# Kernel optimization log

Measured on AMD Instinct MI355X. Metric: run time of the kernel, lower is better.

## Reference

```python
import math
import jax, jax.numpy as jnp
import numpy as np

B_, L_, D_, N_, R_ = 4, 1024, 1024, 16, 64  # batch, seq, n_embd(=dim_inner), d_state, dt_rank


def setup_inputs() -> dict:
    key = jax.random.key(0)
    ks = jax.random.split(key, 6)
    s = lambda k, shp: jax.random.normal(k, shp, jnp.float32) * 0.02
    return {
        "x": jax.random.normal(ks[0], (B_, L_, D_), jnp.float32),
        "ln1_w": jnp.ones((D_,), jnp.float32),
        "ln2_w": jnp.ones((D_,), jnp.float32),
        "W_dbc": s(ks[1], (R_ + 2 * N_, D_)),   # x -> [delta_lowrank, B, C]
        "W_dt": s(ks[2], (D_, R_)),              # dt_rank -> dim_inner
        "b_dt": jnp.zeros((D_,), jnp.float32),
        "A_log": jnp.log(jnp.broadcast_to(jnp.arange(1, N_ + 1, dtype=jnp.float32), (D_, N_))),
        "Dp": jnp.ones((D_,), jnp.float32),      # skip-connection D parameter
        "W_fc": s(ks[3], (4 * D_, D_)),
        "W_proj": s(ks[4], (D_, 4 * D_)),
    }


def _layernorm(x, w):
    mu = jnp.mean(x, -1, keepdims=True)
    xc = x - mu
    var = jnp.mean(xc * xc, -1, keepdims=True)
    return xc * jax.lax.rsqrt(var + 1e-5) * w


def _new_gelu(x):
    c = math.sqrt(2.0 / math.pi)
    return 0.5 * x * (1.0 + jnp.tanh(c * (x + 0.044715 * x * x * x)))


def _ssm(x, W_dbc, W_dt, b_dt, A_log, Dp):
    # x: (b, l, d) with d == dim_inner == n_embd
    dbc = jnp.einsum("bld,ed->ble", x, W_dbc)                # (b,l,R+2N)
    delta, Bm, Cm = jnp.split(dbc, [R_, R_ + N_], axis=-1)
    delta = jax.nn.softplus(jnp.einsum("blr,dr->bld", delta, W_dt) + b_dt)  # (b,l,d)
    A = -jnp.exp(A_log)                                       # (d,n)
    dA = jnp.exp(delta[..., None] * A)                        # (b,l,d,n) discretized A
    dBx = (delta * x)[..., None] * Bm[:, :, None, :]          # (b,l,d,n) discretized B*x

    # h_t = dA_t * h_{t-1} + dBx_t  -> parallel first-order linear scan
    def combine(e1, e2):
        a1, b1 = e1
        a2, b2 = e2
        return a2 * a1, a2 * b1 + b2

    _, hs = jax.lax.associative_scan(combine, (dA, dBx), axis=1)
    y = jnp.einsum("bldn,bln->bld", hs, Cm)
    return y + x * Dp


def reference(x, ln1_w, ln2_w, W_dbc, W_dt, b_dt, A_log, Dp, W_fc, W_proj):
    h = jax.nn.softplus(_layernorm(x, ln1_w))
    h = h + _ssm(h, W_dbc, W_dt, b_dt, A_log, Dp)
    m = _layernorm(h, ln2_w)
    m = _new_gelu(jnp.einsum("bld,fd->blf", m, W_fc))
    m = jnp.einsum("blf,df->bld", m, W_proj)
    return h + m
```

## Files before the change

kernel.cpp:

```cpp
#include <hip/hip_runtime.h>
#include <cstdint>
#include <cstddef>

typedef unsigned short u16;
typedef unsigned int u32;
typedef __attribute__((ext_vector_type(8))) short short8;
typedef __attribute__((ext_vector_type(4))) float floatx4;
typedef __attribute__((ext_vector_type(4))) u16 u16x4;
typedef __attribute__((ext_vector_type(4))) u32 u32x4;

#define DEV static __device__ __forceinline__

DEV u16 f2b(float f){ u32 u = __float_as_uint(f); u32 r = u + 0x7fffu + ((u>>16)&1u); return (u16)(r>>16); }
DEV float softplusf(float z){ return fmaxf(z,0.f) + log1pf(__expf(-fabsf(z))); }
DEV float fast_tanhf(float u){ float e = __expf(2.f*u); return 1.f - 2.f/(e+1.f); }
DEV float geluf(float x){ float u = 0.7978845608028654f*(x + 0.044715f*x*x*x); return 0.5f*x*(1.f+fast_tanhf(u)); }

DEV void async_copy16(const void* gp, void* lp){
  __builtin_amdgcn_global_load_lds((const __attribute__((address_space(1))) u32*)gp,
                                   (__attribute__((address_space(3))) u32*)lp, 16, 0, 0);
}

DEV u32 ldsoff(const void* p){
  return (u32)(size_t)(const __attribute__((address_space(3))) char*)p;
}

DEV void ds_read128x4(u32 base, short8* dst){
  u32x4 r0, r1, r2, r3;
  asm volatile("ds_read_b128 %0, %4 offset:0\n\t"
               "ds_read_b128 %1, %4 offset:1024\n\t"
               "ds_read_b128 %2, %4 offset:2048\n\t"
               "ds_read_b128 %3, %4 offset:3072"
               : "=&v"(r0), "=&v"(r1), "=&v"(r2), "=&v"(r3)
               : "v"(base));
  union { u32x4 u; short8 s; } c0, c1, c2, c3;
  c0.u = r0; c1.u = r1; c2.u = r2; c3.u = r3;
  dst[0] = c0.s; dst[1] = c1.s; dst[2] = c2.s; dst[3] = c3.s;
}

__global__ __launch_bounds__(256)
void prep_ln1(const float* __restrict__ Wdbc, const float* __restrict__ Wdt,
              const float* __restrict__ Wfc, const float* __restrict__ Wproj,
              u16* __restrict__ dbc_b, u16* __restrict__ dt_b,
              u16* __restrict__ fc_b, u16* __restrict__ pj_b,
              const float* __restrict__ x, const float* __restrict__ ln1w,
              float* __restrict__ h0f, u16* __restrict__ h0b)
{
  __shared__ float red[8];
  int bx = blockIdx.x, tid = threadIdx.x;
  if (bx < 8384){
    int i = bx*256 + tid;
    const float* src; u16* dst; int j;
    if (i < 32768){
      int e = i*4, r = e >> 10;
      if (r >= 96){ u16x4 z = {0,0,0,0}; *(u16x4*)(dbc_b + e) = z; return; }
      src = Wdbc; dst = dbc_b; j = i;
    } else if (i < 49152){ src = Wdt;   dst = dt_b; j = i - 32768; }
    else if (i < 1097728){ src = Wfc;   dst = fc_b; j = i - 49152; }
    else                 { src = Wproj; dst = pj_b; j = i - 1097728; }
    float4 v = ((const float4*)src)[j];
    u16x4 o = { f2b(v.x), f2b(v.y), f2b(v.z), f2b(v.w) };
    *(u16x4*)(dst + j*4) = o;
    return;
  }
  int row = bx - 8384;
  const float4* xr = (const float4*)(x + (size_t)row*1024);
  float4 v = xr[tid];
  float s1 = v.x+v.y+v.z+v.w;
  float s2 = v.x*v.x+v.y*v.y+v.z*v.z+v.w*v.w;
  #pragma unroll
  for (int m=1;m<64;m<<=1){ s1 += __shfl_xor(s1,m); s2 += __shfl_xor(s2,m); }
  int wv = tid>>6;
  if ((tid&63)==0){ red[wv]=s1; red[4+wv]=s2; }
  __syncthreads();
  s1 = red[0]+red[1]+red[2]+red[3];
  s2 = red[4]+red[5]+red[6]+red[7];
  float mu  = s1*(1.f/1024.f);
  float var = s2*(1.f/1024.f) - mu*mu;
  float rstd = rsqrtf(var + 1e-5f);
  float4 wv4 = ((const float4*)ln1w)[tid];
  float o0 = softplusf((v.x-mu)*rstd*wv4.x);
  float o1 = softplusf((v.y-mu)*rstd*wv4.y);
  float o2 = softplusf((v.z-mu)*rstd*wv4.z);
  float o3 = softplusf((v.w-mu)*rstd*wv4.w);
  ((float4*)(h0f + (size_t)row*1024))[tid] = make_float4(o0,o1,o2,o3);
  u16x4 ob = { f2b(o0), f2b(o1), f2b(o2), f2b(o3) };
  *(u16x4*)(h0b + (size_t)row*1024 + tid*4) = ob;
}

__global__ void dbc_post(const float* __restrict__ p, u16* __restrict__ delta_in,
                         float* __restrict__ BCf){
  int e = blockIdx.x*256 + threadIdx.x;
  int t = e >> 7, c = e & 127;
  float s = 0.f;
  #pragma unroll
  for (int z=0;z<8;z++) s += p[(size_t)z*524288 + e];
  if (c < 64)      delta_in[t*64 + c] = f2b(s);
  else if (c < 96) BCf[t*32 + (c-64)] = s;
}

__global__ void proj_reduce(const float* __restrict__ p, float* __restrict__ out){
  int i = blockIdx.x*256 + threadIdx.x;
  float4 a = ((const float4*)p)[i];
  float4 b = ((const float4*)(p + (size_t) 4194304))[i];
  float4 c = ((const float4*)(p + (size_t) 8388608))[i];
  float4 d = ((const float4*)(p + (size_t)12582912))[i];
  float4 r = ((float4*)out)[i];
  float4 o = make_float4(a.x+b.x+c.x+d.x+r.x, a.y+b.y+c.y+d.y+r.y,
                         a.z+b.z+c.z+d.z+r.z, a.w+b.w+c.w+d.w+r.w);
  ((float4*)out)[i] = o;
}

__global__ __launch_bounds__(256)
void ln2_kernel(const float* __restrict__ x, const float* __restrict__ w,
                u16* __restrict__ outb)
{
  int row = blockIdx.x, tid = threadIdx.x;
  const float4* xr = (const float4*)(x + (size_t)row*1024);
  float4 v = xr[tid];
  float s1 = v.x+v.y+v.z+v.w;
  float s2 = v.x*v.x+v.y*v.y+v.z*v.z+v.w*v.w;
  #pragma unroll
  for (int m=1;m<64;m<<=1){ s1 += __shfl_xor(s1,m); s2 += __shfl_xor(s2,m); }
  __shared__ float red[8];
  int wv = tid>>6;
  if ((tid&63)==0){ red[wv]=s1; red[4+wv]=s2; }
  __syncthreads();
  s1 = red[0]+red[1]+red[2]+red[3];
  s2 = red[4]+red[5]+red[6]+red[7];
  float mu  = s1*(1.f/1024.f);
  float var = s2*(1.f/1024.f) - mu*mu;
  float rstd = rsqrtf(var + 1e-5f);
  float4 wv4 = ((const float4*)w)[tid];
  u16x4 ob = { f2b((v.x-mu)*rstd*wv4.x), f2b((v.y-mu)*rstd*wv4.y),
               f2b((v.z-mu)*rstd*wv4.z), f2b((v.w-mu)*rstd*wv4.w) };
  *(u16x4*)(outb + (size_t)row*1024 + tid*4) = ob;
}

template<int EPI, int SWZ>
__global__ __launch_bounds__(256)
void gemm_bt(const u16* __restrict__ A, int lda,
             const u16* __restrict__ B, int ldb, int K,
             float* __restrict__ outF, u16* __restrict__ outB, int ldo,
             const float* __restrict__ bias, size_t zstr)
{
  __shared__ u16 sA[128*32];
  __shared__ u16 sB[128*32];
  const int tid = threadIdx.x;
  int m_blk, n_blk, zb;
  if (SWZ == 0){ n_blk = blockIdx.x; m_blk = blockIdx.y; zb = blockIdx.z; }
  else if (SWZ == 1){
    int b = blockIdx.x, xcd = b & 7, local = b >> 3;
    m_blk = (xcd>>2)*16 + (local & 15);
    n_blk = (xcd&3)*8 + (local >> 4);
    zb = 0;
  } else {
    int b = blockIdx.x, xcd = b & 7, local = b >> 3;
    m_blk = (xcd>>1)*8 + (local & 7);
    n_blk = local >> 3;
    zb = xcd & 1;
  }
  const int m0 = m_blk*128, n0 = n_blk*128;
  const int kstart = zb * K;
  const int wave = tid>>6, lane = tid&63;
  const int wm = (wave>>1)*64, wn = (wave&1)*64;
  const int lr = lane&15, quad = lane>>4;

  floatx4 acc[4][4];
  #pragma unroll
  for (int i=0;i<4;i++)
    #pragma unroll
    for (int j=0;j<4;j++){ floatx4 z = {0.f,0.f,0.f,0.f}; acc[i][j]=z; }

  const int r0 = tid>>2;
  const int kc8 = (((tid&3) ^ ((tid>>3)&3)))*8;
  const int sswz = ((lr>>1)&3);
  for (int k0=kstart; k0<kstart+K; k0+=32){
    __syncthreads();
    async_copy16(A + (size_t)(m0+r0)*lda    + k0+kc8, &sA[(size_t)tid*8]);
    async_copy16(A + (size_t)(m0+64+r0)*lda + k0+kc8, &sA[(size_t)(tid+256)*8]);
    async_copy16(B + (size_t)(n0+r0)*ldb    + k0+kc8, &sB[(size_t)tid*8]);
    async_copy16(B + (size_t)(n0+64+r0)*ldb + k0+kc8, &sB[(size_t)(tid+256)*8]);
    __syncthreads();
    short8 af[4], bf[4];
    #pragma unroll
    for (int i=0;i<4;i++){
      af[i] = *(const short8*)&sA[(wm+i*16+lr)*32 + (quad^sswz)*8];
      bf[i] = *(const short8*)&sB[(wn+i*16+lr)*32 + (quad^sswz)*8];
    }
    #pragma unroll
    for (int i=0;i<4;i++)
      #pragma unroll
      for (int j=0;j<4;j++)
        acc[i][j] = __builtin_amdgcn_mfma_f32_16x16x32_bf16(af[i], bf[j], acc[i][j], 0,0,0);
  }
  #pragma unroll
  for (int i=0;i<4;i++){
    #pragma unroll
    for (int j=0;j<4;j++){
      #pragma unroll
      for (int r=0;r<4;r++){
        int gr = m0 + wm + i*16 + quad*4 + r;
        int gc = n0 + wn + j*16 + lr;
        float v = acc[i][j][r];
        size_t o = (size_t)gr*ldo + gc;
        if (EPI==1)      outF[o] = softplusf(v + bias[gc]);
        else if (EPI==2) outB[o] = f2b(geluf(v));
        else             outF[zstr*zb + o] = v;
      }
    }
  }
}

template<int EPI, int SWZ>
__global__ __launch_bounds__(512, 2)
void gemm256(const u16* __restrict__ A, int lda,
             const u16* __restrict__ B, int ldb, int K,
             float* __restrict__ outF, u16* __restrict__ outB, int ldo, size_t zstr)
{
  __shared__ u16 sA[2][4][4096];
  __shared__ u16 sB[2][4][4096];
  const int tid = threadIdx.x;
  int m_blk, n_blk, zb;
  if (SWZ == 3){
    int b = blockIdx.x, xcd = b & 7, local = b >> 3;
    m_blk = (xcd>>2)*8 + (local & 7);
    n_blk = (xcd&3)*4 + (local >> 3);
    zb = 0;
  } else {
    int b = blockIdx.x, xcd = b & 7, local = b >> 3;
    zb    = xcd >> 1;
    m_blk = (xcd&1)*8 + (local & 7);
    n_blk = local >> 3;
  }
  const int m0 = m_blk*256, n0 = n_blk*256;
  const int kstart = zb*K;
  const int wave = tid>>6, lane = tid&63;
  const int mq = wave>>2, nq = wave&3;
  const int lr = lane&15, quad = lane>>4;
  const int sswz = (lr>>1)&3;

  const int srow = tid>>2;
  const int scol = ((tid&3) ^ ((tid>>3)&3))*8;
  const u16* pa = A + (size_t)(m0 + srow)*lda + scol;
  const u16* pb = B + (size_t)(n0 + srow)*ldb + scol;
  u16* la = (u16*)sA + tid*8;
  u16* lb = (u16*)sB + tid*8;
  const size_t ah128 = (size_t)128*lda;
  const size_t bh128 = (size_t)128*ldb;

  const int a_rd = (mq*64 + lr)*32 + (quad^sswz)*8;
  const int b_rd = ((nq&1)*64 + lr)*32 + (quad^sswz)*8;
  const int bun  = nq>>1;
  const u32 a_rdB = ldsoff(sA) + (u32)(a_rd*2);
  const u32 b_rdB = ldsoff(sB) + (u32)(b_rd*2) + (u32)(bun*8192);

  floatx4 acc[2][4][4];
  #pragma unroll
  for (int h=0;h<2;h++)
    #pragma unroll
    for (int i=0;i<4;i++)
      #pragma unroll
      for (int j=0;j<4;j++){ floatx4 z={0.f,0.f,0.f,0.f}; acc[h][i][j]=z; }

  short8 af[2][4], bf[2][4];

#define STG_A(NB,KS,H,KT) async_copy16(pa + (size_t)(H)*ah128 + (size_t)((KT) + (KS)*32), \
                                       la + (NB)*16384 + ((KS)*2+(H))*4096)
#define STG_B(NB,KS,H,KT) async_copy16(pb + (size_t)(H)*bh128 + (size_t)((KT) + (KS)*32), \
                                       lb + (NB)*16384 + ((KS)*2+(H))*4096)

#define PH(MFS, MBS, AH, PRBUF, PRKS, PRAH, PRB, VM, LG, STMTS)               \
  {                                                                           \
    STMTS;                                                                    \
    asm volatile("s_waitcnt vmcnt(" VM ")" ::: "memory");                     \
    __builtin_amdgcn_s_barrier();                                             \
    ds_read128x4(a_rdB + (PRBUF)*32768u + (PRKS)*16384u + (PRAH)*8192u,       \
                 af[(MFS)^1]);                                                \
    if (PRB)                                                                  \
      ds_read128x4(b_rdB + (PRBUF)*32768u + (PRKS)*16384u, bf[(MBS)^1]);      \
    asm volatile("s_waitcnt lgkmcnt(" LG ")" ::: "memory");                   \
    __builtin_amdgcn_sched_barrier(0);                                        \
    __builtin_amdgcn_s_setprio(1);                                            \
    _Pragma("unroll")                                                         \
    for (int i_=0;i_<4;i_++)                                                  \
      _Pragma("unroll")                                                       \
      for (int j_=0;j_<4;j_++)                                                \
        acc[AH][i_][j_] = __builtin_amdgcn_mfma_f32_16x16x32_bf16(            \
            af[MFS][i_], bf[MBS][j_], acc[AH][i_][j_], 0,0,0);                \
    __builtin_amdgcn_s_setprio(0);                                            \
  }

  STG_A(0,0,0,kstart); STG_B(0,0,0,kstart);
  STG_B(0,0,1,kstart); STG_A(0,0,1,kstart);
  STG_B(0,1,0,kstart); STG_B(0,1,1,kstart);
  STG_A(0,1,0,kstart); STG_A(0,1,1,kstart);
  asm volatile("s_waitcnt vmcnt(5)" ::: "memory");
  __builtin_amdgcn_s_barrier();
  ds_read128x4(a_rdB, af[0]);
  ds_read128x4(b_rdB, bf[0]);

  const int NT = K >> 6;
  for (int t=0; t<NT; t+=2){
    const int ka = kstart + (t+1)*64;
    const int kb = (t+2 < NT) ? (kstart + (t+2)*64) : kstart;
    PH(0,0,0, 0,0,1,0, "6","4", STG_A(1,0,0,ka); STG_B(1,0,0,ka));
    PH(1,0,1, 0,1,0,1, "5","8", STG_B(1,0,1,ka); STG_A(1,0,1,ka));
    PH(0,1,0, 0,1,1,0, "6","4", STG_B(1,1,0,ka); STG_B(1,1,1,ka));
    PH(1,1,1, 1,0,0,1, "5","8", STG_A(1,1,0,ka); STG_A(1,1,1,ka));
    PH(0,0,0, 1,0,1,0, "6","4", STG_A(0,0,0,kb); STG_B(0,0,0,kb));
    PH(1,0,1, 1,1,0,1, "5","8", STG_B(0,0,1,kb); STG_A(0,0,1,kb));
    PH(0,1,0, 1,1,1,0, "6","4", STG_B(0,1,0,kb); STG_B(0,1,1,kb));
    PH(1,1,1, 0,0,0,1, "5","8", STG_A(0,1,0,kb); STG_A(0,1,1,kb));
  }

#undef PH
#undef STG_A
#undef STG_B

  #pragma unroll
  for (int h=0;h<2;h++){
    #pragma unroll
    for (int i=0;i<4;i++){
      #pragma unroll
      for (int j=0;j<4;j++){
        #pragma unroll
        for (int r=0;r<4;r++){
          int gr = m0 + h*128 + mq*64 + i*16 + quad*4 + r;
          int gc = n0 + nq*64 + j*16 + lr;
          float v = acc[h][i][j][r];
          size_t o = (size_t)gr*ldo + gc;
          if (EPI==2) outB[o] = f2b(geluf(v));
          else        outF[zstr*zb + o] = v;
        }
      }
    }
  }
}

__global__ __launch_bounds__(256)
void scan_p1(const float* __restrict__ delta, const float* __restrict__ h0f,
             const float* __restrict__ BCf, const float* __restrict__ A_log,
             float* __restrict__ Pbuf, float* __restrict__ Sbuf)
{
  int blk = blockIdx.x;
  int d = (blk & 3)*256 + threadIdx.x;
  int c = (blk >> 2) & 31;
  int b = blk >> 7;
  float a2[16], h[16], P[16];
  #pragma unroll
  for (int n=0;n<16;n++){ a2[n] = -__expf(A_log[d*16+n]) * 1.44269504f; h[n]=0.f; P[n]=1.f; }
  int t0 = c*32;
  const float* dptr = delta + ((size_t)(b*1024 + t0))*1024 + d;
  const float* xptr = h0f   + ((size_t)(b*1024 + t0))*1024 + d;
  const float* bc   = BCf   + ((size_t)(b*1024 + t0))*32;
  #pragma unroll 4
  for (int t=0;t<32;t++){
    float dlt = dptr[t*1024];
    float xv  = xptr[t*1024];
    float dx = dlt*xv;
    #pragma unroll
    for (int n=0;n<16;n++){
      float dA = exp2f(dlt*a2[n]);
      h[n] = dA*h[n] + dx*bc[t*32+n];
      P[n] *= dA;
    }
  }
  size_t base = ((size_t)((b*32 + c)*16))*1024 + d;
  #pragma unroll
  for (int n=0;n<16;n++){ Pbuf[base + (size_t)n*1024] = P[n]; Sbuf[base + (size_t)n*1024] = h[n]; }
}

__global__ __launch_bounds__(256)
void scan_p2(const float* __restrict__ Pbuf, const float* __restrict__ Sbuf,
             float* __restrict__ Hbuf)
{
  int blk = blockIdx.x;
  int d = (blk & 3)*256 + threadIdx.x;
  int n = (blk >> 2) & 15;
  int b = blk >> 6;
  float H = 0.f;
  for (int c=0;c<32;c++){
    size_t idx = ((size_t)((b*32 + c)*16 + n))*1024 + d;
    float P = Pbuf[idx], S = Sbuf[idx];
    Hbuf[idx] = H;
    H = P*H + S;
  }
}

__global__ __launch_bounds__(256)
void scan_p3(const float* __restrict__ delta, const float* __restrict__ h0f,
             const float* __restrict__ BCf, const float* __restrict__ A_log,
             const float* __restrict__ Hbuf, const float* __restrict__ Dp,
             float* __restrict__ outp)
{
  int blk = blockIdx.x;
  int d = (blk & 3)*256 + threadIdx.x;
  int c = (blk >> 2) & 31;
  int b = blk >> 7;
  float a2[16], h[16];
  size_t hb = ((size_t)((b*32 + c)*16))*1024 + d;
  #pragma unroll
  for (int n=0;n<16;n++){
    a2[n] = -__expf(A_log[d*16+n]) * 1.44269504f;
    h[n] = Hbuf[hb + (size_t)n*1024];
  }
  float dpv = 1.f + Dp[d];
  int t0 = c*32;
  const float* dptr = delta + ((size_t)(b*1024 + t0))*1024 + d;
  const float* xptr = h0f   + ((size_t)(b*1024 + t0))*1024 + d;
  const float* bc   = BCf   + ((size_t)(b*1024 + t0))*32;
  float* wptr = outp + ((size_t)(b*1024 + t0))*1024 + d;
  #pragma unroll 4
  for (int t=0;t<32;t++){
    float dlt = dptr[t*1024];
    float xv  = xptr[t*1024];
    float dx = dlt*xv;
    float y = 0.f;
    #pragma unroll
    for (int n=0;n<16;n++){
      float dA = exp2f(dlt*a2[n]);
      h[n] = dA*h[n] + dx*bc[t*32+n];
      y += h[n]*bc[t*32+16+n];
    }
    wptr[t*1024] = xv*dpv + y;
  }
}

extern "C" void kernel_launch(void* const* d_in, const int* in_sizes, int n_in,
                              void* d_out, int out_size, void* d_ws, size_t ws_size,
                              hipStream_t stream)
{
  const float* x    = (const float*)d_in[0];
  const float* ln1w = (const float*)d_in[1];
  const float* ln2w = (const float*)d_in[2];
  const float* Wdbc = (const float*)d_in[3];
  const float* Wdt  = (const float*)d_in[4];
  const float* bdt  = (const float*)d_in[5];
  const float* Alog = (const float*)d_in[6];
  const float* Dp   = (const float*)d_in[7];
  const float* Wfc  = (const float*)d_in[8];
  const float* Wproj= (const float*)d_in[9];
  float* out = (float*)d_out;

  char* ws = (char*)d_ws;
  size_t off = 0;
  auto carve = [&](size_t bytes)->char*{ char* p = ws + off; off += (bytes + 255) & ~(size_t)255; return p; };
  const size_t T = 4096;
  float* h0f   = (float*)carve(T*1024*4);
  float* dlt   = (float*)carve(T*1024*4);
  float* Pbuf  = (float*)carve((size_t)4*32*16*1024*4);
  float* Sbuf  = (float*)carve((size_t)4*32*16*1024*4);
  float* Hbuf  = (float*)carve((size_t)4*32*16*1024*4);
  float* pad_  = (float*)carve((size_t)4*32*16*1024*4);
  float* BCf   = (float*)carve(T*32*4);
  u16*   h0b   = (u16*)  carve(T*1024*2);
  u16*   m0b   = (u16*)  carve(T*1024*2);
  u16*   g_b   = (u16*)  carve(T*4096*2);
  u16*   din_b = (u16*)  carve(T*64*2);
  u16*   Wdbc_b= (u16*)  carve((size_t)128*1024*2);
  u16*   Wdt_b = (u16*)  carve((size_t)1024*64*2);
  u16*   Wfc_b = (u16*)  carve((size_t)4096*1024*2);
  u16*   Wpj_b = (u16*)  carve((size_t)1024*4096*2);
  float* dbc_p  = Hbuf;
  float* proj_p = dlt;
  (void)pad_; (void)ws_size; (void)in_sizes; (void)n_in; (void)out_size;

  prep_ln1<<<12480, 256, 0, stream>>>(Wdbc, Wdt, Wfc, Wproj,
                                      Wdbc_b, Wdt_b, Wfc_b, Wpj_b,
                                      x, ln1w, h0f, h0b);

  gemm_bt<4,0><<<dim3(1,32,8), 256, 0, stream>>>(h0b, 1024, Wdbc_b, 1024, 128,
                                                 dbc_p, nullptr, 128, nullptr, (size_t)T*128);
  dbc_post<<<2048, 256, 0, stream>>>(dbc_p, din_b, BCf);

  gemm_bt<1,0><<<dim3(8,32), 256, 0, stream>>>(din_b, 64, Wdt_b, 64, 64,
                                               dlt, nullptr, 1024, bdt, 0);

  scan_p1<<<512, 256, 0, stream>>>(dlt, h0f, BCf, Alog, Pbuf, Sbuf);
  scan_p2<<<256, 256, 0, stream>>>(Pbuf, Sbuf, Hbuf);
  scan_p3<<<512, 256, 0, stream>>>(dlt, h0f, BCf, Alog, Hbuf, Dp, out);

  ln2_kernel<<<4096, 256, 0, stream>>>(out, ln2w, m0b);

  gemm256<2,3><<<256, 512, 0, stream>>>(m0b, 1024, Wfc_b, 1024, 1024,
                                        nullptr, g_b, 4096, 0);

  gemm256<4,4><<<256, 512, 0, stream>>>(g_b, 4096, Wpj_b, 4096, 1024,
                                        proj_p, nullptr, 1024, (size_t)T*1024);
  proj_reduce<<<4096, 256, 0, stream>>>(proj_p, out);
}
```

Before: 322.2 us.

## Fuse split-K proj reduction into GEMM epilogue via atomic tile counters

Removes the separate proj_reduce kernel by having the last-arriving split-K block of each output tile sum the other three partial buffers plus the residual and write the final output. Earlier blocks write their partials and signal completion through per-tile counters, which ln2_kernel resets. This avoids a launch, one partial write and the extra read pass from the last block's own partial. The cost is a spin-wait that relies on all 256 blocks being co-resident, and atomic/fence overhead.

```diff
diff --git a/kernel.cpp b/kernel.cpp
--- a/kernel.cpp
+++ b/kernel.cpp
@@ -99,23 +99,12 @@
   else if (c < 96) BCf[t*32 + (c-64)] = s;
 }
 
-__global__ void proj_reduce(const float* __restrict__ p, float* __restrict__ out){
-  int i = blockIdx.x*256 + threadIdx.x;
-  float4 a = ((const float4*)p)[i];
-  float4 b = ((const float4*)(p + (size_t) 4194304))[i];
-  float4 c = ((const float4*)(p + (size_t) 8388608))[i];
-  float4 d = ((const float4*)(p + (size_t)12582912))[i];
-  float4 r = ((float4*)out)[i];
-  float4 o = make_float4(a.x+b.x+c.x+d.x+r.x, a.y+b.y+c.y+d.y+r.y,
-                         a.z+b.z+c.z+d.z+r.z, a.w+b.w+c.w+d.w+r.w);
-  ((float4*)out)[i] = o;
-}
-
 __global__ __launch_bounds__(256)
 void ln2_kernel(const float* __restrict__ x, const float* __restrict__ w,
-                u16* __restrict__ outb)
+                u16* __restrict__ outb, u32* __restrict__ cz)
 {
   int row = blockIdx.x, tid = threadIdx.x;
+  if (row == 0 && tid < 128) cz[tid] = 0u;
   const float4* xr = (const float4*)(x + (size_t)row*1024);
   float4 v = xr[tid];
   float s1 = v.x+v.y+v.z+v.w;
@@ -216,10 +205,12 @@
 __global__ __launch_bounds__(512, 2)
 void gemm256(const u16* __restrict__ A, int lda,
              const u16* __restrict__ B, int ldb, int K,
-             float* __restrict__ outF, u16* __restrict__ outB, int ldo, size_t zstr)
+             float* __restrict__ outF, u16* __restrict__ outB, int ldo, size_t zstr,
+             float* __restrict__ pbuf, u32* __restrict__ cnta, u32* __restrict__ cntd)
 {
   __shared__ u16 sA[2][4][4096];
   __shared__ u16 sB[2][4][4096];
+  __shared__ u32 s_old;
   const int tid = threadIdx.x;
   int m_blk, n_blk, zb;
   if (SWZ == 3){
@@ -318,22 +309,62 @@
 #undef STG_A
 #undef STG_B
 
-  #pragma unroll
-  for (int h=0;h<2;h++){
-    #pragma unroll
-    for (int i=0;i<4;i++){
+  if (EPI==2){
+    #pragma unroll
+    for (int h=0;h<2;h++)
       #pragma unroll
-      for (int j=0;j<4;j++){
+      for (int i=0;i<4;i++)
         #pragma unroll
-        for (int r=0;r<4;r++){
-          int gr = m0 + h*128 + mq*64 + i*16 + quad*4 + r;
-          int gc = n0 + nq*64 + j*16 + lr;
-          float v = acc[h][i][j][r];
-          size_t o = (size_t)gr*ldo + gc;
-          if (EPI==2) outB[o] = f2b(geluf(v));
-          else        outF[zstr*zb + o] = v;
-        }
+        for (int j=0;j<4;j++)
+          #pragma unroll
+          for (int r=0;r<4;r++){
+            int gr = m0 + h*128 + mq*64 + i*16 + quad*4 + r;
+            int gc = n0 + nq*64 + j*16 + lr;
+            outB[(size_t)gr*ldo + gc] = f2b(geluf(acc[h][i][j][r]));
+          }
+  } else {
+    const int tile = m_blk*4 + n_blk;
+    if (tid==0) s_old = atomicAdd(&cnta[tile], 1u);
+    __syncthreads();
+    if (s_old < 3u){
+      #pragma unroll
+      for (int h=0;h<2;h++)
+        #pragma unroll
+        for (int i=0;i<4;i++)
+          #pragma unroll
+          for (int j=0;j<4;j++)
+            #pragma unroll
+            for (int r=0;r<4;r++){
+              int gr = m0 + h*128 + mq*64 + i*16 + quad*4 + r;
+              int gc = n0 + nq*64 + j*16 + lr;
+              pbuf[zstr*zb + (size_t)gr*ldo + gc] = acc[h][i][j][r];
+            }
+      __syncthreads();
+      if (tid==0){ __threadfence(); atomicAdd(&cntd[tile], 1u); }
+    } else {
+      if (tid==0){
+        while (__hip_atomic_load(&cntd[tile], __ATOMIC_ACQUIRE, __HIP_MEMORY_SCOPE_AGENT) < 3u)
+          __builtin_amdgcn_s_sleep(8);
       }
+      __syncthreads();
+      __threadfence();
+      #pragma unroll
+      for (int h=0;h<2;h++)
+        #pragma unroll
+        for (int i=0;i<4;i++)
+          #pragma unroll
+          for (int j=0;j<4;j++)
+            #pragma unroll
+            for (int r=0;r<4;r++){
+              int gr = m0 + h*128 + mq*64 + i*16 + quad*4 + r;
+              int gc = n0 + nq*64 + j*16 + lr;
+              size_t o = (size_t)gr*ldo + gc;
+              float s = acc[h][i][j][r] + outF[o];
+              #pragma unroll
+              for (int z=0;z<4;z++)
+                if (z != zb) s += pbuf[zstr*z + o];
+              outF[o] = s;
+            }
     }
   }
 }
@@ -462,6 +493,7 @@
   u16*   Wdt_b = (u16*)  carve((size_t)1024*64*2);
   u16*   Wfc_b = (u16*)  carve((size_t)4096*1024*2);
   u16*   Wpj_b = (u16*)  carve((size_t)1024*4096*2);
+  u32*   cnt   = (u32*)  carve(512);
   float* dbc_p  = Hbuf;
   float* proj_p = dlt;
   (void)pad_; (void)ws_size; (void)in_sizes; (void)n_in; (void)out_size;
@@ -481,12 +513,12 @@
   scan_p2<<<256, 256, 0, stream>>>(Pbuf, Sbuf, Hbuf);
   scan_p3<<<512, 256, 0, stream>>>(dlt, h0f, BCf, Alog, Hbuf, Dp, out);
 
-  ln2_kernel<<<4096, 256, 0, stream>>>(out, ln2w, m0b);
+  ln2_kernel<<<4096, 256, 0, stream>>>(out, ln2w, m0b, cnt);
 
   gemm256<2,3><<<256, 512, 0, stream>>>(m0b, 1024, Wfc_b, 1024, 1024,
-                                        nullptr, g_b, 4096, 0);
+                                        nullptr, g_b, 4096, 0, nullptr, nullptr, nullptr);
 
   gemm256<4,4><<<256, 512, 0, stream>>>(g_b, 4096, Wpj_b, 4096, 1024,
-                                        proj_p, nullptr, 1024, (size_t)T*1024);
-  proj_reduce<<<4096, 256, 0, stream>>>(proj_p, out);
-}
+                                        out, nullptr, 1024, (size_t)T*1024,
+                                        proj_p, cnt, cnt + 64);
+}
```

New measurement: 487.5 us. 51.3% more time.
